# Optimization experiments

Hardware: AMD Instinct MI355X
Metric: run time of the kernel (lower is better)

Reference implementation:

```python
import jax, jax.numpy as jnp
import numpy as np

B, C, H, W = 8, 512, 32, 32
NH, DH = 8, 64          # num_heads, head_dim (C = NH*DH)
GROUPS, EPS = 32, 1e-5


def group_norm(x, gamma, beta):
    b, c, h, w = x.shape
    xg = x.reshape(b, GROUPS, c // GROUPS, h, w)
    mu = xg.mean(axis=(2, 3, 4), keepdims=True)
    var = xg.var(axis=(2, 3, 4), keepdims=True)
    xn = ((xg - mu) * jax.lax.rsqrt(var + EPS)).reshape(b, c, h, w)
    return xn * gamma[:, None, None] + beta[:, None, None]


def conv1x1(x, w, b):
    # x: [B,C,H,W], w: [O,C], b: [O]
    return jnp.einsum('bchw,oc->bohw', x, w) + b[:, None, None]


def setup_inputs() -> dict:
    key = jax.random.key(0)
    ks = jax.random.split(key, 5)
    return {
        'x': jax.random.normal(ks[0], (B, C, H, W), jnp.float32),
        'norm_gamma': jnp.ones((C,), jnp.float32),
        'norm_beta': jnp.zeros((C,), jnp.float32),
        'qkv_w': jax.random.normal(ks[1], (3 * C, C), jnp.float32) * (1.0 / np.sqrt(C)),
        'qkv_b': jax.random.normal(ks[2], (3 * C,), jnp.float32) * 0.02,
        'proj_w': jax.random.normal(ks[3], (C, C), jnp.float32) * (1.0 / np.sqrt(C)),
        'proj_b': jax.random.normal(ks[4], (C,), jnp.float32) * 0.02,
    }


def reference(x, norm_gamma, norm_beta, qkv_w, qkv_b, proj_w, proj_b):
    scale = DH ** -0.5
    h = group_norm(x, norm_gamma, norm_beta)
    qkv = conv1x1(h, qkv_w, qkv_b)                       # [B,3C,H,W]
    qkv = qkv.reshape(B, 3, NH, DH, H * W)
    qkv = jnp.transpose(qkv, (1, 0, 2, 4, 3))            # [3,B,NH,HW,DH]
    q, k, v = qkv[0], qkv[1], qkv[2]
    attn = jnp.einsum('bhid,bhjd->bhij', q, k) * scale   # [B,NH,HW,HW]
    attn = jax.nn.softmax(attn, axis=-1)
    h = jnp.einsum('bhij,bhjd->bhid', attn, v)           # [B,NH,HW,DH]
    # faithful to torch: direct row-major reshape [B,NH,HW,DH] -> [B,C,H,W]
    h = h.reshape(B, C, H, W)
    h = conv1x1(h, proj_w, proj_b)
    return x + h
```

## Files before the change

### kernel.cpp

```cpp
#include <hip/hip_runtime.h>


typedef float  f32x4  __attribute__((ext_vector_type(4)));
typedef __bf16 bf16x8 __attribute__((ext_vector_type(8)));
typedef __bf16 bf16x4 __attribute__((ext_vector_type(4)));

#define MFMA(a, b, c) __builtin_amdgcn_mfma_f32_16x16x32_bf16(a, b, c, 0, 0, 0)

__device__ __forceinline__ void async16(const __bf16* g, __bf16* l) {
  __builtin_amdgcn_global_load_lds((const __attribute__((address_space(1))) void*)g,
                                   (__attribute__((address_space(3))) void*)l, 16, 0, 0);
}

__device__ __forceinline__ int chk(int n, int c) {
  return ((((n >> 6) * 16 + (c >> 5)) * 4 + ((c >> 3) & 3)) * 512) + (n & 63) * 8 + (c & 7);
}

__global__ __launch_bounds__(256) void cvt2_k(const float* __restrict__ qw, __bf16* __restrict__ dq,
                                              const float* __restrict__ pw, __bf16* __restrict__ dp) {
  int i = (blockIdx.x * 256 + threadIdx.x) * 4;
  const float* src = (i < 786432) ? qw : pw;
  __bf16* dst = (i < 786432) ? dq : dp;
  int j = (i < 786432) ? i : (i - 786432);
  int m = j >> 9, k = j & 511;
  float4 v = *(const float4*)(src + j);
  bf16x4 o;
  o[0] = (__bf16)v.x; o[1] = (__bf16)v.y; o[2] = (__bf16)v.z; o[3] = (__bf16)v.w;
  *(bf16x4*)(dst + chk(m, k)) = o;
}

__global__ __launch_bounds__(512) void groupnorm_k(const float* __restrict__ x,
                                                   const float* __restrict__ gamma,
                                                   const float* __restrict__ beta,
                                                   __bf16* __restrict__ Hout) {
  __shared__ __bf16 xs[16 * 1032];
  __shared__ float  red[16];
  __shared__ float  ga[16], be[16], stat[2];
  const int tid = threadIdx.x;
  const int w = tid >> 6, l = tid & 63;
  const int bg = blockIdx.x, b = bg >> 5, g = bg & 31, c0 = g * 16;
  const float* xg = x + b * 524288 + c0 * 1024;

  float sum = 0.f, sq = 0.f;
#pragma unroll
  for (int p = 0; p < 8; p++) {
    int idx = p * 2048 + tid * 4;
    float4 v = *(const float4*)(xg + idx);
    int c = idx >> 10, s = idx & 1023;
    bf16x4 o;
    o[0] = (__bf16)v.x; o[1] = (__bf16)v.y; o[2] = (__bf16)v.z; o[3] = (__bf16)v.w;
    *(bf16x4*)(&xs[c * 1032 + s]) = o;
    sum += v.x + v.y + v.z + v.w;
    sq  += v.x * v.x + v.y * v.y + v.z * v.z + v.w * v.w;
  }
#pragma unroll
  for (int o = 32; o > 0; o >>= 1) { sum += __shfl_down(sum, o); sq += __shfl_down(sq, o); }
  if (l == 0) { red[w * 2] = sum; red[w * 2 + 1] = sq; }
  __syncthreads();
  if (tid == 0) {
    float S = 0.f, Q = 0.f;
#pragma unroll
    for (int i = 0; i < 8; i++) { S += red[i * 2]; Q += red[i * 2 + 1]; }
    float mean = S * (1.f / 16384.f);
    float var  = Q * (1.f / 16384.f) - mean * mean;
    stat[0] = mean; stat[1] = rsqrtf(var + 1e-5f);
  }
  if (tid < 16) { ga[tid] = gamma[c0 + tid]; be[tid] = beta[c0 + tid]; }
  __syncthreads();
  const float mean = stat[0], rstd = stat[1];
#pragma unroll
  for (int p = 0; p < 2; p++) {
    int s = p * 512 + tid;
    int n = b * 1024 + s;
    bf16x8 o0, o1;
#pragma unroll
    for (int c = 0; c < 8; c++) {
      float f = (float)xs[c * 1032 + s];
      o0[c] = (__bf16)((f - mean) * rstd * ga[c] + be[c]);
    }
#pragma unroll
    for (int c = 8; c < 16; c++) {
      float f = (float)xs[c * 1032 + s];
      o1[c - 8] = (__bf16)((f - mean) * rstd * ga[c] + be[c]);
    }
    *(bf16x8*)(Hout + chk(n, c0)) = o0;
    *(bf16x8*)(Hout + chk(n, c0 + 8)) = o1;
  }
}

__global__ __launch_bounds__(256) void gemm_qkv_k(const __bf16* __restrict__ W,
                                                  const float* __restrict__ bias,
                                                  const __bf16* __restrict__ H,
                                                  __bf16* __restrict__ qbuf,
                                                  __bf16* __restrict__ kbuf,
                                                  __bf16* __restrict__ vt) {
  __shared__ union {
    struct { __bf16 a[2][4096]; __bf16 b[2][4096]; } ab;
    __bf16 cs[128 * 136];
  } lds;
  const int tid = threadIdx.x;
  const int w = tid >> 6, l = tid & 63, quad = l >> 4, li = l & 15;
  const int wr = w >> 1, wc = w & 1;
  const int mblk = blockIdx.x >> 6, nblk = blockIdx.x & 63;
  const int m0 = mblk * 128, n0 = nblk * 128;

  f32x4 acc[4][4];
#pragma unroll
  for (int i = 0; i < 4; i++)
#pragma unroll
    for (int j = 0; j < 4; j++) acc[i][j] = f32x4{0.f, 0.f, 0.f, 0.f};

  const __bf16* Ag = W + (((m0 >> 6) * 16) * 4 + w) * 512 + l * 8;
  const __bf16* Bg = H + (((n0 >> 6) * 16) * 4 + w) * 512 + l * 8;
  const int halfA = 16 * 4 * 512;

  async16(Ag,         &lds.ab.a[0][w * 1024]);
  async16(Ag + halfA, &lds.ab.a[0][w * 1024 + 512]);
  async16(Bg,         &lds.ab.b[0][w * 1024]);
  async16(Bg + halfA, &lds.ab.b[0][w * 1024 + 512]);

#pragma unroll 1
  for (int kt = 0; kt < 16; kt++) {
    int cur = kt & 1, nxt = cur ^ 1;
    __syncthreads();
    if (kt < 15) {
      int ko = (kt + 1) * 2048;
      async16(Ag + ko,          &lds.ab.a[nxt][w * 1024]);
      async16(Ag + halfA + ko,  &lds.ab.a[nxt][w * 1024 + 512]);
      async16(Bg + ko,          &lds.ab.b[nxt][w * 1024]);
      async16(Bg + halfA + ko,  &lds.ab.b[nxt][w * 1024 + 512]);
    }
    bf16x8 af[4], bfr[4];
#pragma unroll
    for (int i = 0; i < 4; i++)
      af[i] = *(const bf16x8*)(&lds.ab.a[cur][quad * 1024 + (wr * 64 + i * 16 + li) * 8]);
#pragma unroll
    for (int i = 0; i < 4; i++)
      bfr[i] = *(const bf16x8*)(&lds.ab.b[cur][quad * 1024 + (wc * 64 + i * 16 + li) * 8]);
#pragma unroll
    for (int i = 0; i < 4; i++)
#pragma unroll
      for (int j = 0; j < 4; j++) acc[i][j] = MFMA(af[i], bfr[j], acc[i][j]);
  }

  const int t = m0 >> 9;
  const int cbase = m0 & 511;
  __syncthreads();
#pragma unroll
  for (int mi = 0; mi < 4; mi++) {
    int olocal = wr * 64 + mi * 16 + quad * 4;
    float bs[4];
#pragma unroll
    for (int r = 0; r < 4; r++) bs[r] = bias[m0 + olocal + r];
#pragma unroll
    for (int ni = 0; ni < 4; ni++) {
      int nlocal = wc * 64 + ni * 16 + li;
      bf16x4 pk;
#pragma unroll
      for (int r = 0; r < 4; r++) {
        float f = acc[mi][ni][r] + bs[r];
        if (t == 0) f *= 0.180336880f;
        pk[r] = (__bf16)f;
      }
      *(bf16x4*)(&lds.cs[nlocal * 136 + olocal]) = pk;
    }
  }
  __syncthreads();
  const int bb = n0 >> 10, s0 = n0 & 1023;
  if (t < 2) {
    __bf16* dst = (t == 0) ? qbuf : kbuf;
    const int nh0 = cbase >> 6;
#pragma unroll
    for (int p = 0; p < 8; p++) {
      int idx = p * 256 + tid;
      int oc = idx & 15, nloc = idx >> 4;
      uint4 val = *(const uint4*)(&lds.cs[nloc * 136 + oc * 8]);
      int bh = bb * 8 + nh0 + (oc >> 3);
      int s = s0 + nloc, d0 = (oc & 7) * 8;
      *(uint4*)(dst + (((bh * 16 + (s >> 6)) * 8 + (d0 >> 3)) * 64 + (s & 63)) * 8) = val;
    }
  } else {
#pragma unroll
    for (int p = 0; p < 8; p++) {
      int idx = p * 256 + tid;
      int o = idx & 127, ng = idx >> 7;
      int c = cbase + o, nh2 = c >> 6, d = c & 63;
      int bh = bb * 8 + nh2;
      int j0 = s0 + ng * 8;
      bf16x8 vv;
#pragma unroll
      for (int jj = 0; jj < 8; jj++) vv[jj] = lds.cs[(ng * 8 + jj) * 136 + o];
      *(bf16x8*)(vt + (((bh * 16 + (j0 >> 6)) * 8 + ((j0 >> 3) & 7)) * 64 + d) * 8) = vv;
    }
  }
}

__global__ __launch_bounds__(256) void attn_k(const __bf16* __restrict__ qb,
                                              const __bf16* __restrict__ kb,
                                              const __bf16* __restrict__ vt,
                                              __bf16* __restrict__ pin) {
  __shared__ __bf16 KC[2][4096];
  __shared__ __bf16 VC[2][4096];
  __shared__ union { __bf16 q[4096]; __bf16 p[4096]; __bf16 o[4096]; } PQ;
  const int tid = threadIdx.x;
  const int w = tid >> 6, l = tid & 63, quad = l >> 4, li = l & 15;
  const int x = blockIdx.x;
  const int qt = (x >> 3) & 15;
  const int bh = (x & 7) | ((x >> 7) << 3);
  const int b = bh >> 3, nh = bh & 7;
  const __bf16* Qg = qb + bh * 65536;
  const __bf16* Kg = kb + bh * 65536;
  const __bf16* Vg = vt + bh * 65536;

#pragma unroll
  for (int p = 0; p < 2; p++) {
    int ch = w + 4 * p;
    async16(Qg + ((qt * 8 + ch) * 64) * 8 + l * 8, &PQ.q[ch * 512 + l * 8]);
    async16(Kg + (ch * 64) * 8 + l * 8,            &KC[0][ch * 512 + l * 8]);
    async16(Vg + (ch * 64) * 8 + l * 8,            &VC[0][ch * 512 + l * 8]);
  }
  __syncthreads();
  bf16x8 qf[2];
#pragma unroll
  for (int ks = 0; ks < 2; ks++)
    qf[ks] = *(const bf16x8*)(&PQ.q[(ks * 4 + quad) * 512 + (w * 16 + li) * 8]);
  __syncthreads();

  float lsum = 0.f;
  f32x4 oacc[4];
#pragma unroll
  for (int dt = 0; dt < 4; dt++) oacc[dt] = f32x4{0.f, 0.f, 0.f, 0.f};

#pragma unroll 1
  for (int kv = 0; kv < 16; kv++) {
    int cur = kv & 1, nxt = cur ^ 1;
    if (kv < 15) {
#pragma unroll
      for (int p = 0; p < 2; p++) {
        int ch = w + 4 * p;
        async16(Kg + (((kv + 1) * 8 + ch) * 64) * 8 + l * 8, &KC[nxt][ch * 512 + l * 8]);
        async16(Vg + (((kv + 1) * 8 + ch) * 64) * 8 + l * 8, &VC[nxt][ch * 512 + l * 8]);
      }
    }

    f32x4 st[4];
#pragma unroll
    for (int jt = 0; jt < 4; jt++) st[jt] = f32x4{0.f, 0.f, 0.f, 0.f};
#pragma unroll
    for (int ks = 0; ks < 2; ks++)
#pragma unroll
      for (int jt = 0; jt < 4; jt++) {
        bf16x8 kf = *(const bf16x8*)(&KC[cur][(ks * 4 + quad) * 512 + (jt * 16 + li) * 8]);
        st[jt] = MFMA(kf, qf[ks], st[jt]);
      }

#pragma unroll
    for (int jt = 0; jt < 4; jt++) {
      f32x4 v = st[jt];
      bf16x4 pk;
      float p0 = __builtin_amdgcn_exp2f(v[0]);
      float p1 = __builtin_amdgcn_exp2f(v[1]);
      float p2 = __builtin_amdgcn_exp2f(v[2]);
      float p3 = __builtin_amdgcn_exp2f(v[3]);
      lsum += (p0 + p1) + (p2 + p3);
      pk[0] = (__bf16)p0; pk[1] = (__bf16)p1; pk[2] = (__bf16)p2; pk[3] = (__bf16)p3;
      *(bf16x4*)(&PQ.p[w * 1024 + (jt * 2 + (quad >> 1)) * 128 + li * 8 + (quad & 1) * 4]) = pk;
    }

#pragma unroll
    for (int ks2 = 0; ks2 < 2; ks2++) {
      bf16x8 pf = *(const bf16x8*)(&PQ.p[w * 1024 + (ks2 * 4 + quad) * 128 + li * 8]);
#pragma unroll
      for (int dt = 0; dt < 4; dt++) {
        bf16x8 vf = *(const bf16x8*)(&VC[cur][(ks2 * 4 + quad) * 512 + (dt * 16 + li) * 8]);
        oacc[dt] = MFMA(pf, vf, oacc[dt]);
      }
    }
    __syncthreads();
  }

  lsum += __shfl_xor(lsum, 16);
  lsum += __shfl_xor(lsum, 32);
  const float inv = 1.f / lsum;
#pragma unroll
  for (int r = 0; r < 4; r++) {
    float ib = __shfl(inv, quad * 4 + r);
#pragma unroll
    for (int dt = 0; dt < 4; dt++)
      PQ.o[((quad * 4 + r) * 64 + dt * 16 + li) * 4 + w] = (__bf16)(oacc[dt][r] * ib);
  }
  __syncthreads();
  __bf16* Pg = pin + (nh * 8 + (qt >> 1)) * 65536 + (qt & 1) * 4 + b * 8192;
#pragma unroll
  for (int p = 0; p < 4; p++) {
    int n = p * 256 + tid;
    bf16x4 ov = *(const bf16x4*)(&PQ.o[n * 4]);
    *(bf16x4*)(Pg + n * 8) = ov;
  }
}

__global__ __launch_bounds__(256) void gemm_proj_k(const __bf16* __restrict__ W,
                                                   const float* __restrict__ bias,
                                                   const __bf16* __restrict__ P,
                                                   const float* __restrict__ x,
                                                   float* __restrict__ out) {
  __shared__ __bf16 AL[2][2048];
  __shared__ __bf16 BL[2][4096];
  const int tid = threadIdx.x;
  const int w = tid >> 6, l = tid & 63, quad = l >> 4, li = l & 15;
  const int wr = w >> 1, wc = w & 1;
  const int mblk = blockIdx.x >> 6, nblk = blockIdx.x & 63;
  const int m0 = mblk * 64, n0 = nblk * 128;

  f32x4 acc[2][4];
#pragma unroll
  for (int i = 0; i < 2; i++)
#pragma unroll
    for (int j = 0; j < 4; j++) acc[i][j] = f32x4{0.f, 0.f, 0.f, 0.f};

  const __bf16* Ag = W + ((mblk * 16) * 4 + w) * 512 + l * 8;
  const __bf16* Bg = P + w * 65536 + (n0 + l) * 8;

  async16(Ag,       &AL[0][w * 512]);
  async16(Bg,       &BL[0][w * 1024]);
  async16(Bg + 512, &BL[0][w * 1024 + 512]);

#pragma unroll 1
  for (int kt = 0; kt < 16; kt++) {
    int cur = kt & 1, nxt = cur ^ 1;
    __syncthreads();
    if (kt < 15) {
      int koA = (kt + 1) * 2048;
      int koB = (kt + 1) * 262144;
      async16(Ag + koA,       &AL[nxt][w * 512]);
      async16(Bg + koB,       &BL[nxt][w * 1024]);
      async16(Bg + koB + 512, &BL[nxt][w * 1024 + 512]);
    }
    bf16x8 af[2], bfr[4];
#pragma unroll
    for (int i = 0; i < 2; i++)
      af[i] = *(const bf16x8*)(&AL[cur][quad * 512 + (wr * 32 + i * 16 + li) * 8]);
#pragma unroll
    for (int j = 0; j < 4; j++)
      bfr[j] = *(const bf16x8*)(&BL[cur][quad * 1024 + (wc * 64 + j * 16 + li) * 8]);
#pragma unroll
    for (int i = 0; i < 2; i++)
#pragma unroll
      for (int j = 0; j < 4; j++) acc[i][j] = MFMA(af[i], bfr[j], acc[i][j]);
  }

  const int bb = n0 >> 10;
#pragma unroll
  for (int mi = 0; mi < 2; mi++) {
    int o = m0 + wr * 32 + mi * 16 + quad * 4;
    float bs[4];
#pragma unroll
    for (int r = 0; r < 4; r++) bs[r] = bias[o + r];
#pragma unroll
    for (int ni = 0; ni < 4; ni++) {
      int n = n0 + wc * 64 + ni * 16 + li;
      int s = n & 1023;
#pragma unroll
      for (int r = 0; r < 4; r++) {
        int a = (bb * 512 + o + r) * 1024 + s;
        out[a] = acc[mi][ni][r] + bs[r] + x[a];
      }
    }
  }
}

extern "C" void kernel_launch(void* const* d_in, const int* in_sizes, int n_in,
                              void* d_out, int out_size, void* d_ws, size_t ws_size,
                              hipStream_t stream) {
  const float* x      = (const float*)d_in[0];
  const float* gamma  = (const float*)d_in[1];
  const float* beta   = (const float*)d_in[2];
  const float* qkv_w  = (const float*)d_in[3];
  const float* qkv_b  = (const float*)d_in[4];
  const float* proj_w = (const float*)d_in[5];
  const float* proj_b = (const float*)d_in[6];

  __bf16* ws   = (__bf16*)d_ws;
  __bf16* H    = ws;
  __bf16* qbuf = ws + 4194304;
  __bf16* kbuf = ws + 8388608;
  __bf16* vt   = ws + 12582912;
  __bf16* wq   = ws + 16777216;
  __bf16* wp   = ws + 17563648;

  cvt2_k<<<1024, 256, 0, stream>>>(qkv_w, wq, proj_w, wp);
  groupnorm_k<<<256, 512, 0, stream>>>(x, gamma, beta, H);
  gemm_qkv_k<<<768, 256, 0, stream>>>(wq, qkv_b, H, qbuf, kbuf, vt);
  attn_k<<<1024, 256, 0, stream>>>(qbuf, kbuf, vt, H);
  gemm_proj_k<<<512, 256, 0, stream>>>(wp, proj_b, H, x, (float*)d_out);
}
```

Measured before the change: 141.4 us.

## Switch attention to 32x32 MFMA with 128-row query tiles; fuse prep kernels

The attention kernel now uses 32x32x16 bf16 MFMA tiles, with each wave covering 32 query rows, so a block handles 128 query rows and the grid is halved. Each K/V tile is therefore reused across more queries. Q fragments are loaded straight from global into registers, P is staged through an XOR-swizzled LDS buffer, and the output is written with wider 16-byte stores. Separately, the weight bf16 conversion and the groupnorm kernel are merged into one launch to save a launch and let the two run concurrently. The trade-off is more register pressure from the 16-wide accumulators and fewer blocks available to fill the GPU.

Result: no change. 143.2 us (+1.3%).

```diff
diff --git a/kernel.cpp b/kernel.cpp
--- a/kernel.cpp
+++ b/kernel.cpp
@@ -2,10 +2,13 @@
 
 
 typedef float  f32x4  __attribute__((ext_vector_type(4)));
+typedef float  f32x16 __attribute__((ext_vector_type(16)));
 typedef __bf16 bf16x8 __attribute__((ext_vector_type(8)));
 typedef __bf16 bf16x4 __attribute__((ext_vector_type(4)));
-
-#define MFMA(a, b, c) __builtin_amdgcn_mfma_f32_16x16x32_bf16(a, b, c, 0, 0, 0)
+typedef __bf16 bf16x2 __attribute__((ext_vector_type(2)));
+
+#define MFMA(a, b, c)   __builtin_amdgcn_mfma_f32_16x16x32_bf16(a, b, c, 0, 0, 0)
+#define MFMA32(a, b, c) __builtin_amdgcn_mfma_f32_32x32x16_bf16(a, b, c, 0, 0, 0)
 
 __device__ __forceinline__ void async16(const __bf16* g, __bf16* l) {
   __builtin_amdgcn_global_load_lds((const __attribute__((address_space(1))) void*)g,
@@ -16,27 +19,30 @@
   return ((((n >> 6) * 16 + (c >> 5)) * 4 + ((c >> 3) & 3)) * 512) + (n & 63) * 8 + (c & 7);
 }
 
-__global__ __launch_bounds__(256) void cvt2_k(const float* __restrict__ qw, __bf16* __restrict__ dq,
+__global__ __launch_bounds__(512) void prep_k(const float* __restrict__ x,
+                                              const float* __restrict__ gamma,
+                                              const float* __restrict__ beta,
+                                              __bf16* __restrict__ Hout,
+                                              const float* __restrict__ qw, __bf16* __restrict__ dq,
                                               const float* __restrict__ pw, __bf16* __restrict__ dp) {
-  int i = (blockIdx.x * 256 + threadIdx.x) * 4;
-  const float* src = (i < 786432) ? qw : pw;
-  __bf16* dst = (i < 786432) ? dq : dp;
-  int j = (i < 786432) ? i : (i - 786432);
-  int m = j >> 9, k = j & 511;
-  float4 v = *(const float4*)(src + j);
-  bf16x4 o;
-  o[0] = (__bf16)v.x; o[1] = (__bf16)v.y; o[2] = (__bf16)v.z; o[3] = (__bf16)v.w;
-  *(bf16x4*)(dst + chk(m, k)) = o;
-}
-
-__global__ __launch_bounds__(512) void groupnorm_k(const float* __restrict__ x,
-                                                   const float* __restrict__ gamma,
-                                                   const float* __restrict__ beta,
-                                                   __bf16* __restrict__ Hout) {
   __shared__ __bf16 xs[16 * 1032];
   __shared__ float  red[16];
   __shared__ float  ga[16], be[16], stat[2];
   const int tid = threadIdx.x;
+
+  if (blockIdx.x >= 256) {
+    int i = ((blockIdx.x - 256) * 512 + tid) * 4;
+    const float* src = (i < 786432) ? qw : pw;
+    __bf16* dst = (i < 786432) ? dq : dp;
+    int j = (i < 786432) ? i : (i - 786432);
+    int m = j >> 9, k = j & 511;
+    float4 v = *(const float4*)(src + j);
+    bf16x4 o;
+    o[0] = (__bf16)v.x; o[1] = (__bf16)v.y; o[2] = (__bf16)v.z; o[3] = (__bf16)v.w;
+    *(bf16x4*)(dst + chk(m, k)) = o;
+    return;
+  }
+
   const int w = tid >> 6, l = tid & 63;
   const int bg = blockIdx.x, b = bg >> 5, g = bg & 31, c0 = g * 16;
   const float* xg = x + b * 524288 + c0 * 1024;
@@ -201,12 +207,12 @@
                                               __bf16* __restrict__ pin) {
   __shared__ __bf16 KC[2][4096];
   __shared__ __bf16 VC[2][4096];
-  __shared__ union { __bf16 q[4096]; __bf16 p[4096]; __bf16 o[4096]; } PQ;
+  __shared__ __bf16 PO[8192];
   const int tid = threadIdx.x;
-  const int w = tid >> 6, l = tid & 63, quad = l >> 4, li = l & 15;
+  const int w = tid >> 6, l = tid & 63, hi = l >> 5, i32 = l & 31;
   const int x = blockIdx.x;
-  const int qt = (x >> 3) & 15;
-  const int bh = (x & 7) | ((x >> 7) << 3);
+  const int qt = (x >> 3) & 7;
+  const int bh = (x & 7) | ((x >> 6) << 3);
   const int b = bh >> 3, nh = bh & 7;
   const __bf16* Qg = qb + bh * 65536;
   const __bf16* Kg = kb + bh * 65536;
@@ -215,21 +221,24 @@
 #pragma unroll
   for (int p = 0; p < 2; p++) {
     int ch = w + 4 * p;
-    async16(Qg + ((qt * 8 + ch) * 64) * 8 + l * 8, &PQ.q[ch * 512 + l * 8]);
-    async16(Kg + (ch * 64) * 8 + l * 8,            &KC[0][ch * 512 + l * 8]);
-    async16(Vg + (ch * 64) * 8 + l * 8,            &VC[0][ch * 512 + l * 8]);
-  }
-  __syncthreads();
-  bf16x8 qf[2];
-#pragma unroll
-  for (int ks = 0; ks < 2; ks++)
-    qf[ks] = *(const bf16x8*)(&PQ.q[(ks * 4 + quad) * 512 + (w * 16 + li) * 8]);
-  __syncthreads();
-
+    async16(Kg + ch * 512 + l * 8, &KC[0][ch * 512 + l * 8]);
+    async16(Vg + ch * 512 + l * 8, &VC[0][ch * 512 + l * 8]);
+  }
+
+  const int s = qt * 128 + w * 32 + i32;
+  bf16x8 qf[4];
+#pragma unroll
+  for (int ks = 0; ks < 4; ks++)
+    qf[ks] = *(const bf16x8*)(Qg + ((s >> 6) * 8 + ks * 2 + hi) * 512 + (s & 63) * 8);
+
+  __syncthreads();
+
+  const int swz = (i32 & 7) << 4;
+  char* Pw = (char*)PO + w * 4096;
   float lsum = 0.f;
-  f32x4 oacc[4];
-#pragma unroll
-  for (int dt = 0; dt < 4; dt++) oacc[dt] = f32x4{0.f, 0.f, 0.f, 0.f};
+  f32x16 oacc[2];
+#pragma unroll
+  for (int r = 0; r < 16; r++) { oacc[0][r] = 0.f; oacc[1][r] = 0.f; }
 
 #pragma unroll 1
   for (int kv = 0; kv < 16; kv++) {
@@ -238,64 +247,72 @@
 #pragma unroll
       for (int p = 0; p < 2; p++) {
         int ch = w + 4 * p;
-        async16(Kg + (((kv + 1) * 8 + ch) * 64) * 8 + l * 8, &KC[nxt][ch * 512 + l * 8]);
-        async16(Vg + (((kv + 1) * 8 + ch) * 64) * 8 + l * 8, &VC[nxt][ch * 512 + l * 8]);
-      }
-    }
-
-    f32x4 st[4];
-#pragma unroll
-    for (int jt = 0; jt < 4; jt++) st[jt] = f32x4{0.f, 0.f, 0.f, 0.f};
-#pragma unroll
-    for (int ks = 0; ks < 2; ks++)
-#pragma unroll
-      for (int jt = 0; jt < 4; jt++) {
-        bf16x8 kf = *(const bf16x8*)(&KC[cur][(ks * 4 + quad) * 512 + (jt * 16 + li) * 8]);
-        st[jt] = MFMA(kf, qf[ks], st[jt]);
-      }
-
-#pragma unroll
-    for (int jt = 0; jt < 4; jt++) {
-      f32x4 v = st[jt];
-      bf16x4 pk;
-      float p0 = __builtin_amdgcn_exp2f(v[0]);
-      float p1 = __builtin_amdgcn_exp2f(v[1]);
-      float p2 = __builtin_amdgcn_exp2f(v[2]);
-      float p3 = __builtin_amdgcn_exp2f(v[3]);
-      lsum += (p0 + p1) + (p2 + p3);
-      pk[0] = (__bf16)p0; pk[1] = (__bf16)p1; pk[2] = (__bf16)p2; pk[3] = (__bf16)p3;
-      *(bf16x4*)(&PQ.p[w * 1024 + (jt * 2 + (quad >> 1)) * 128 + li * 8 + (quad & 1) * 4]) = pk;
-    }
-
-#pragma unroll
-    for (int ks2 = 0; ks2 < 2; ks2++) {
-      bf16x8 pf = *(const bf16x8*)(&PQ.p[w * 1024 + (ks2 * 4 + quad) * 128 + li * 8]);
-#pragma unroll
-      for (int dt = 0; dt < 4; dt++) {
-        bf16x8 vf = *(const bf16x8*)(&VC[cur][(ks2 * 4 + quad) * 512 + (dt * 16 + li) * 8]);
-        oacc[dt] = MFMA(pf, vf, oacc[dt]);
+        async16(Kg + (kv + 1) * 4096 + ch * 512 + l * 8, &KC[nxt][ch * 512 + l * 8]);
+        async16(Vg + (kv + 1) * 4096 + ch * 512 + l * 8, &VC[nxt][ch * 512 + l * 8]);
+      }
+    }
+
+    f32x16 st[2];
+#pragma unroll
+    for (int r = 0; r < 16; r++) { st[0][r] = 0.f; st[1][r] = 0.f; }
+#pragma unroll
+    for (int ks = 0; ks < 4; ks++) {
+#pragma unroll
+      for (int jt = 0; jt < 2; jt++) {
+        bf16x8 kf = *(const bf16x8*)(&KC[cur][(ks * 2 + hi) * 512 + (jt * 32 + i32) * 8]);
+        st[jt] = MFMA32(kf, qf[ks], st[jt]);
+      }
+    }
+
+#pragma unroll
+    for (int jt = 0; jt < 2; jt++) {
+#pragma unroll
+      for (int q2 = 0; q2 < 4; q2++) {
+        float p0 = __builtin_amdgcn_exp2f(st[jt][q2 * 4 + 0]);
+        float p1 = __builtin_amdgcn_exp2f(st[jt][q2 * 4 + 1]);
+        float p2 = __builtin_amdgcn_exp2f(st[jt][q2 * 4 + 2]);
+        float p3 = __builtin_amdgcn_exp2f(st[jt][q2 * 4 + 3]);
+        lsum += (p0 + p1) + (p2 + p3);
+        bf16x4 pk;
+        pk[0] = (__bf16)p0; pk[1] = (__bf16)p1; pk[2] = (__bf16)p2; pk[3] = (__bf16)p3;
+        *(bf16x4*)(Pw + ((i32 * 128 + jt * 64 + q2 * 16 + hi * 8) ^ swz)) = pk;
+      }
+    }
+
+#pragma unroll
+    for (int js = 0; js < 4; js++) {
+      bf16x8 pf = *(const bf16x8*)(Pw + ((i32 * 128 + js * 32 + hi * 16) ^ swz));
+#pragma unroll
+      for (int dt = 0; dt < 2; dt++) {
+        bf16x8 vf = *(const bf16x8*)(&VC[cur][(js * 2 + hi) * 512 + (dt * 32 + i32) * 8]);
+        oacc[dt] = MFMA32(pf, vf, oacc[dt]);
       }
     }
     __syncthreads();
   }
 
-  lsum += __shfl_xor(lsum, 16);
   lsum += __shfl_xor(lsum, 32);
   const float inv = 1.f / lsum;
-#pragma unroll
-  for (int r = 0; r < 4; r++) {
-    float ib = __shfl(inv, quad * 4 + r);
-#pragma unroll
-    for (int dt = 0; dt < 4; dt++)
-      PQ.o[((quad * 4 + r) * 64 + dt * 16 + li) * 4 + w] = (__bf16)(oacc[dt][r] * ib);
-  }
-  __syncthreads();
-  __bf16* Pg = pin + (nh * 8 + (qt >> 1)) * 65536 + (qt & 1) * 4 + b * 8192;
+
+#pragma unroll
+  for (int dt = 0; dt < 2; dt++) {
+#pragma unroll
+    for (int r = 0; r < 8; r++) {
+      int ilo = (r & 3) + 8 * (r >> 2) + 4 * hi;
+      float iblo = __shfl(inv, ilo);
+      float ibhi = __shfl(inv, ilo + 16);
+      bf16x2 ov;
+      ov[0] = (__bf16)(oacc[dt][r]     * iblo);
+      ov[1] = (__bf16)(oacc[dt][r + 8] * ibhi);
+      *(bf16x2*)((char*)PO + (ilo * 64 + dt * 32 + i32) * 16 + w * 4) = ov;
+    }
+  }
+  __syncthreads();
+  __bf16* Pg = pin + (nh * 8 + qt) * 65536 + b * 8192;
 #pragma unroll
   for (int p = 0; p < 4; p++) {
-    int n = p * 256 + tid;
-    bf16x4 ov = *(const bf16x4*)(&PQ.o[n * 4]);
-    *(bf16x4*)(Pg + n * 8) = ov;
+    int idx = p * 256 + tid;
+    *(bf16x8*)(Pg + idx * 8) = *(const bf16x8*)((const char*)PO + idx * 16);
   }
 }
 
@@ -388,9 +405,8 @@
   __bf16* wq   = ws + 16777216;
   __bf16* wp   = ws + 17563648;
 
-  cvt2_k<<<1024, 256, 0, stream>>>(qkv_w, wq, proj_w, wp);
-  groupnorm_k<<<256, 512, 0, stream>>>(x, gamma, beta, H);
+  prep_k<<<768, 512, 0, stream>>>(x, gamma, beta, H, qkv_w, wq, proj_w, wp);
   gemm_qkv_k<<<768, 256, 0, stream>>>(wq, qkv_b, H, qbuf, kbuf, vt);
-  attn_k<<<1024, 256, 0, stream>>>(qbuf, kbuf, vt, H);
+  attn_k<<<512, 256, 0, stream>>>(qbuf, kbuf, vt, H);
   gemm_proj_k<<<512, 256, 0, stream>>>(wp, proj_b, H, x, (float*)d_out);
 }
```
